# Kernel tuning notes

Hardware: AMD Instinct MI355X
Metric: run time of the kernel (lower is better)

Reference implementation:

```python
import jax, jax.numpy as jnp
import numpy as np

IN_FEATURES = 4096
OUT_FEATURES = 4096
N_TOKENS = 4096  # batch*seq rows fed through the linear layer


def setup_inputs() -> dict:
    key = jax.random.key(0)
    kx, kw, kb = jax.random.split(key, 3)
    x = jax.random.normal(kx, (N_TOKENS, IN_FEATURES), dtype=jnp.float32)
    # kaiming_uniform-like init scale for weight, uniform bias as in reset_parameters
    bound_w = float(np.sqrt(6.0 / ((1.0 + 5.0) * IN_FEATURES)))  # kaiming_uniform a=sqrt(5)
    weight = jax.random.uniform(kw, (OUT_FEATURES, IN_FEATURES), dtype=jnp.float32,
                                minval=-bound_w, maxval=bound_w)
    bound_b = float(1.0 / np.sqrt(IN_FEATURES))
    bias = jax.random.uniform(kb, (OUT_FEATURES,), dtype=jnp.float32,
                              minval=-bound_b, maxval=bound_b)
    return {"x": x, "weight": weight, "bias": bias}


def reference(x, weight, bias):
    # quantize_weights(bits=8): scale = 127 / max|W|; W_int8 = int8-cast(W*scale)
    # (numpy int8 cast truncates toward zero). The cutlass int8 GEMM computes
    # x_int8 @ W_int8^T, dequantized by 1/scale, plus bias. Math equivalent:
    # y = x @ (trunc(W*scale)/scale)^T + bias
    scale = 127.0 / jnp.max(jnp.abs(weight))
    w_q = jnp.clip(jnp.trunc(weight * scale), -127.0, 127.0)  # emulated int8 weight
    w_deq = w_q / scale                                       # [out, in]
    return jnp.einsum('ti,oi->to', x, w_deq) + bias           # [tokens, out]
```

## Files before the change

### kernel.cpp

```cpp
#include <hip/hip_runtime.h>
#include <stdint.h>

#define M_DIM 4096
#define N_DIM 4096
#define K_DIM 4096

typedef int i32x4 __attribute__((ext_vector_type(4)));

__global__ void prep1_kernel(const float* __restrict__ w,
                             const float* __restrict__ x,
                             float* __restrict__ wpmax,
                             char* __restrict__ xq,
                             float* __restrict__ xsinv) {
    __shared__ float sred[4];
    const int t = threadIdx.x;
    if (blockIdx.x < 2048) {
        int tid = blockIdx.x * 256 + t;
        const int stride = 2048 * 256;
        const int n4 = (N_DIM * K_DIM) / 4;
        const float4* w4 = (const float4*)w;
        float m = 0.f;
        for (int i = tid; i < n4; i += stride) {
            float4 a = w4[i];
            m = fmaxf(m, fmaxf(fmaxf(fabsf(a.x), fabsf(a.y)), fmaxf(fabsf(a.z), fabsf(a.w))));
        }
        for (int off = 32; off > 0; off >>= 1) m = fmaxf(m, __shfl_xor(m, off));
        if ((t & 63) == 0) sred[t >> 6] = m;
        __syncthreads();
        if (t == 0)
            wpmax[blockIdx.x] = fmaxf(fmaxf(sred[0], sred[1]), fmaxf(sred[2], sred[3]));
    } else {
        const int rbase = (blockIdx.x - 2048) * 2;
        #pragma unroll
        for (int r = 0; r < 2; ++r) {
            const int row = rbase + r;
            const float4* xr = (const float4*)(x + (size_t)row * K_DIM);
            float4 v[4];
            float m = 0.f;
            #pragma unroll
            for (int i = 0; i < 4; ++i) {
                v[i] = xr[t * 4 + i];
                m = fmaxf(m, fmaxf(fmaxf(fabsf(v[i].x), fabsf(v[i].y)),
                                   fmaxf(fabsf(v[i].z), fabsf(v[i].w))));
            }
            for (int off = 32; off > 0; off >>= 1) m = fmaxf(m, __shfl_xor(m, off));
            if ((t & 63) == 0) sred[t >> 6] = m;
            __syncthreads();
            m = fmaxf(fmaxf(fmaxf(sred[0], sred[1]), fmaxf(sred[2], sred[3])), 1e-30f);
            if (t == 0) xsinv[row] = m * (1.0f / 127.0f);
            const float scale = 127.0f / m;
            int4 o;
            int* op = (int*)&o;
            #pragma unroll
            for (int i = 0; i < 4; ++i) {
                int a = (int)rintf(v[i].x * scale);
                int b = (int)rintf(v[i].y * scale);
                int c = (int)rintf(v[i].z * scale);
                int d = (int)rintf(v[i].w * scale);
                op[i] = (a & 0xff) | ((b & 0xff) << 8) | ((c & 0xff) << 16) | (d << 24);
            }
            *(int4*)(xq + (size_t)row * K_DIM + t * 16) = o;
            __syncthreads();
        }
    }
}

__global__ void prep2_kernel(const float* __restrict__ w,
                             const float* __restrict__ wpmax,
                             int* __restrict__ wq4,
                             float* __restrict__ wdq_out) {
    __shared__ float sred[4];
    const int t = threadIdx.x;
    float m = 0.f;
    #pragma unroll
    for (int i = 0; i < 8; ++i) m = fmaxf(m, wpmax[t * 8 + i]);
    for (int off = 32; off > 0; off >>= 1) m = fmaxf(m, __shfl_xor(m, off));
    if ((t & 63) == 0) sred[t >> 6] = m;
    __syncthreads();
    const float maxv = fmaxf(fmaxf(sred[0], sred[1]), fmaxf(sred[2], sred[3]));
    const float wscale = 127.0f / maxv;
    if (blockIdx.x == 0 && t == 0) *wdq_out = maxv * (1.0f / 127.0f);

    int tid = blockIdx.x * 256 + t;
    const int stride = 2048 * 256;
    const int n4 = (N_DIM * K_DIM) / 4;
    const float4* w4 = (const float4*)w;
    for (int i = tid; i < n4; i += stride) {
        float4 a = w4[i];
        int w0 = (int)fminf(fmaxf(truncf(a.x * wscale), -127.f), 127.f);
        int w1 = (int)fminf(fmaxf(truncf(a.y * wscale), -127.f), 127.f);
        int w2 = (int)fminf(fmaxf(truncf(a.z * wscale), -127.f), 127.f);
        int w3 = (int)fminf(fmaxf(truncf(a.w * wscale), -127.f), 127.f);
        wq4[i] = (w0 & 0xff) | ((w1 & 0xff) << 8) | ((w2 & 0xff) << 16) | (w3 << 24);
    }
}

#define BAR()   __builtin_amdgcn_s_barrier()
#define FENCE() __builtin_amdgcn_sched_barrier(0)

#define MFMA_I8(ACC, AF, BF) \
    asm("v_mfma_i32_16x16x64_i8 %0, %1, %2, %0" : "+v"(ACC) : "v"(AF), "v"(BF))

__global__ __launch_bounds__(512, 2) void gemm_i8(
    const char* __restrict__ A,
    const char* __restrict__ B,
    const float* __restrict__ wdqp,
    const float* __restrict__ xsinv,
    const float* __restrict__ bias,
    float* __restrict__ C)
{
    __shared__ __align__(16) char sM[131072];

    int bid = (blockIdx.x & 7) * 32 + (blockIdx.x >> 3);
    const int bm = bid >> 4;
    const int bn = bid & 15;

    const int t    = threadIdx.x;
    const int wave = t >> 6;
    const int lane = t & 63;
    const int wm   = wave >> 2;
    const int wn   = wave & 3;

    i32x4 acc[2][2][4][2] = {};

    const int chunk = (((lane >> 4) << 4) ^ ((lane & 7) << 4));
    const int lbA0 = ((lane & 15) << 7) + chunk + wm * 8192;
    const int lbA1 = lbA0 ^ 64;
    const int lbB0 = ((lane & 15) << 7) + chunk + wn * 4096 + 65536;
    const int lbB1 = lbB0 ^ 64;

    const int srow = t >> 3;
    const int cch  = (t & 7) ^ (srow & 7);
    const char* Abase = A + (size_t)(bm * 256 + srow) * K_DIM + cch * 16;
    const char* Bbase = B + (size_t)(bn * 256 + srow) * K_DIM + cch * 16;
    const int wave_lds = wave * 1024;

#define STAGE(SRC, REG, H, KT, BUF) do {                                                \
        const char* _s = SRC + (H) * (128 * K_DIM) + ((KT) << 7);                       \
        char* _d = sM + (REG) + (BUF) * 32768 + (H) * 16384 + wave_lds;                 \
        __builtin_amdgcn_global_load_lds(                                               \
            (const __attribute__((address_space(1))) void*)_s,                          \
            (__attribute__((address_space(3))) void*)_d, 16, 0, 0);                     \
        __builtin_amdgcn_global_load_lds(                                               \
            (const __attribute__((address_space(1))) void*)(_s + (size_t)64 * K_DIM),   \
            (__attribute__((address_space(3))) void*)(_d + 8192), 16, 0, 0);            \
    } while(0)

#define LDA(H, BUF, AF) do {                                                            \
        _Pragma("unroll") for (int mi = 0; mi < 4; ++mi) {                              \
            AF[mi][0] = *(const i32x4*)(sM + (BUF)*32768 + (H)*16384 + mi*2048 + lbA0); \
            AF[mi][1] = *(const i32x4*)(sM + (BUF)*32768 + (H)*16384 + mi*2048 + lbA1); \
        }                                                                               \
    } while(0)

#define LDB(G, BUF, BF) do {                                                            \
        _Pragma("unroll") for (int ni = 0; ni < 2; ++ni) {                              \
            BF[ni][0] = *(const i32x4*)(sM + (BUF)*32768 + (G)*16384 + ni*2048 + lbB0); \
            BF[ni][1] = *(const i32x4*)(sM + (BUF)*32768 + (G)*16384 + ni*2048 + lbB1); \
        }                                                                               \
    } while(0)

#define MMAQ(H, G, AF, BF)                                                              \
        _Pragma("unroll") for (int kk = 0; kk < 2; ++kk)                                \
        _Pragma("unroll") for (int mi = 0; mi < 4; ++mi)                                \
        _Pragma("unroll") for (int ni = 0; ni < 2; ++ni)                                \
            MFMA_I8(acc[H][G][mi][ni], AF[mi][kk], BF[ni][kk]);

#define TILE(BUF, OBUF, KN) do {                                                        \
        LDA(0, BUF, af0); LDB(0, BUF, bf0);                    \
        FENCE();                                                                        \
        LDB(1, BUF, bf1);                                                  \
        STAGE(Abase, 0,     0, KN, OBUF);                                               \
        STAGE(Bbase, 65536, 0, KN, OBUF);                                               \
        STAGE(Abase, 0,     1, KN, OBUF);                                               \
        STAGE(Bbase, 65536, 1, KN, OBUF);                                               \
        LDA(1, BUF, af1);                                                  \
        FENCE();                                                                        \
        __builtin_amdgcn_s_setprio(1);                                                  \
        MMAQ(0, 0, af0, bf0);                                                           \
        MMAQ(0, 1, af0, bf1);                                                           \
        MMAQ(1, 1, af1, bf1);                                                           \
        MMAQ(1, 0, af1, bf0);                                                           \
        __builtin_amdgcn_s_setprio(0);                                                  \
        asm volatile("s_waitcnt vmcnt(0)");              \
        BAR();                                                                          \
        FENCE();                                                                        \
    } while(0)

    STAGE(Abase, 0,     0, 0, 0);
    STAGE(Bbase, 65536, 0, 0, 0);
    STAGE(Abase, 0,     1, 0, 0);
    STAGE(Bbase, 65536, 1, 0, 0);
    asm volatile("s_waitcnt vmcnt(0)");
    BAR();
    FENCE();

    i32x4 af0[4][2], af1[4][2], bf0[2][2], bf1[2][2];

    for (int it = 0; it < 16; ++it) {
        TILE(0, 1, (2 * it + 1) & 31);
        TILE(1, 0, (2 * it + 2) & 31);
    }

    const float wdq = *wdqp;

    #pragma unroll
    for (int h = 0; h < 2; ++h)
    #pragma unroll
    for (int mi = 0; mi < 4; ++mi) {
        const int grow0 = bm * 256 + h * 128 + wm * 64 + mi * 16 + (lane >> 4) * 4;
        float rs[4];
        #pragma unroll
        for (int rg = 0; rg < 4; ++rg) rs[rg] = xsinv[grow0 + rg] * wdq;
        #pragma unroll
        for (int g = 0; g < 2; ++g)
        #pragma unroll
        for (int ni = 0; ni < 2; ++ni) {
            const int gcol = bn * 256 + g * 128 + wn * 32 + ni * 16 + (lane & 15);
            const float bv = bias[gcol];
            #pragma unroll
            for (int rg = 0; rg < 4; ++rg)
                C[(size_t)(grow0 + rg) * N_DIM + gcol] =
                    (float)acc[h][g][mi][ni][rg] * rs[rg] + bv;
        }
    }

#undef STAGE
#undef LDA
#undef LDB
#undef MMAQ
#undef TILE
}

extern "C" void kernel_launch(void* const* d_in, const int* in_sizes, int n_in,
                              void* d_out, int out_size, void* d_ws, size_t ws_size,
                              hipStream_t stream) {
    const float* x    = (const float*)d_in[0];
    const float* w    = (const float*)d_in[1];
    const float* bias = (const float*)d_in[2];
    float* out = (float*)d_out;

    float* wpmax = (float*)d_ws;
    float* wdqp  = (float*)((char*)d_ws + 8192);
    float* xsinv = (float*)((char*)d_ws + 8448);
    char*  xq    = (char*)d_ws + 32768;
    char*  wq    = (char*)d_ws + 32768 + (size_t)M_DIM * K_DIM;

    prep1_kernel<<<4096, 256, 0, stream>>>(w, x, wpmax, xq, xsinv);
    prep2_kernel<<<2048, 256, 0, stream>>>(w, wpmax, (int*)wq, wdqp);

    const int grid = (M_DIM / 256) * (N_DIM / 256);
    gemm_i8<<<grid, 512, 0, stream>>>(xq, wq, wdqp, xsinv, bias, out);
}
```

Baseline: 101.1 us.

## Shrink GEMM tile to 128x256x64 with smaller LDS buffers for higher occupancy

Reworks the int8 GEMM tile from 256x256 with K-step 128 to 128x256 with K-step 64. LDS drops from 128KB to 48KB and launch bounds rise to 4 blocks per CU, so more blocks can be resident and latency is hidden better, and the grid doubles to 512 blocks. The LDS swizzle, staging and fragment-load patterns are rewritten for 64-byte rows. In exchange, each block reuses its data less, global traffic per FLOP goes up, and the K loop runs twice as many barrier-separated steps.

```diff
diff --git a/kernel.cpp b/kernel.cpp
--- a/kernel.cpp
+++ b/kernel.cpp
@@ -101,7 +101,9 @@
 #define MFMA_I8(ACC, AF, BF) \
     asm("v_mfma_i32_16x16x64_i8 %0, %1, %2, %0" : "+v"(ACC) : "v"(AF), "v"(BF))
 
-__global__ __launch_bounds__(512, 2) void gemm_i8(
+#define BUFSZ 24576
+
+__global__ __launch_bounds__(512, 4) void gemm_i8(
     const char* __restrict__ A,
     const char* __restrict__ B,
     const float* __restrict__ wdqp,
@@ -109,9 +111,9 @@
     const float* __restrict__ bias,
     float* __restrict__ C)
 {
-    __shared__ __align__(16) char sM[131072];
-
-    int bid = (blockIdx.x & 7) * 32 + (blockIdx.x >> 3);
+    __shared__ __align__(16) char sM[2 * BUFSZ];
+
+    int bid = (blockIdx.x & 7) * 64 + (blockIdx.x >> 3);
     const int bm = bid >> 4;
     const int bn = bid & 15;
 
@@ -121,114 +123,87 @@
     const int wm   = wave >> 2;
     const int wn   = wave & 3;
 
-    i32x4 acc[2][2][4][2] = {};
-
-    const int chunk = (((lane >> 4) << 4) ^ ((lane & 7) << 4));
-    const int lbA0 = ((lane & 15) << 7) + chunk + wm * 8192;
-    const int lbA1 = lbA0 ^ 64;
-    const int lbB0 = ((lane & 15) << 7) + chunk + wn * 4096 + 65536;
-    const int lbB1 = lbB0 ^ 64;
-
-    const int srow = t >> 3;
-    const int cch  = (t & 7) ^ (srow & 7);
-    const char* Abase = A + (size_t)(bm * 256 + srow) * K_DIM + cch * 16;
+    i32x4 acc[4][4] = {};
+
+    const int chunk = (((lane >> 4) ^ ((lane >> 1) & 3)) << 4);
+    const int lbA = ((lane & 15) << 6) + chunk + wm * 4096;
+    const int lbB = ((lane & 15) << 6) + chunk + wn * 4096 + 8192;
+
+    const int srow = t >> 2;
+    const int cch  = (t & 3) ^ ((t >> 3) & 3);
+    const char* Abase = A + (size_t)(bm * 128 + srow) * K_DIM + cch * 16;
     const char* Bbase = B + (size_t)(bn * 256 + srow) * K_DIM + cch * 16;
     const int wave_lds = wave * 1024;
 
-#define STAGE(SRC, REG, H, KT, BUF) do {                                                \
-        const char* _s = SRC + (H) * (128 * K_DIM) + ((KT) << 7);                       \
-        char* _d = sM + (REG) + (BUF) * 32768 + (H) * 16384 + wave_lds;                 \
+#define STAGE(KT, BUF) do {                                                             \
+        const char* _sa = Abase + ((KT) << 6);                                          \
+        char* _da = sM + (BUF) * BUFSZ + wave_lds;                                      \
         __builtin_amdgcn_global_load_lds(                                               \
-            (const __attribute__((address_space(1))) void*)_s,                          \
-            (__attribute__((address_space(3))) void*)_d, 16, 0, 0);                     \
+            (const __attribute__((address_space(1))) void*)_sa,                         \
+            (__attribute__((address_space(3))) void*)_da, 16, 0, 0);                    \
+        const char* _sb = Bbase + ((KT) << 6);                                          \
+        char* _db = sM + (BUF) * BUFSZ + 8192 + wave_lds;                               \
         __builtin_amdgcn_global_load_lds(                                               \
-            (const __attribute__((address_space(1))) void*)(_s + (size_t)64 * K_DIM),   \
-            (__attribute__((address_space(3))) void*)(_d + 8192), 16, 0, 0);            \
+            (const __attribute__((address_space(1))) void*)_sb,                         \
+            (__attribute__((address_space(3))) void*)_db, 16, 0, 0);                    \
+        __builtin_amdgcn_global_load_lds(                                               \
+            (const __attribute__((address_space(1))) void*)(_sb + (size_t)128 * K_DIM), \
+            (__attribute__((address_space(3))) void*)(_db + 8192), 16, 0, 0);           \
     } while(0)
 
-#define LDA(H, BUF, AF) do {                                                            \
-        _Pragma("unroll") for (int mi = 0; mi < 4; ++mi) {                              \
-            AF[mi][0] = *(const i32x4*)(sM + (BUF)*32768 + (H)*16384 + mi*2048 + lbA0); \
-            AF[mi][1] = *(const i32x4*)(sM + (BUF)*32768 + (H)*16384 + mi*2048 + lbA1); \
-        }                                                                               \
+#define LDAB(BUF) do {                                                                  \
+        _Pragma("unroll") for (int mi = 0; mi < 4; ++mi)                                \
+            af[mi] = *(const i32x4*)(sM + (BUF)*BUFSZ + mi*1024 + lbA);                 \
+        _Pragma("unroll") for (int ni = 0; ni < 4; ++ni)                                \
+            bf[ni] = *(const i32x4*)(sM + (BUF)*BUFSZ + ni*1024 + lbB);                 \
     } while(0)
 
-#define LDB(G, BUF, BF) do {                                                            \
-        _Pragma("unroll") for (int ni = 0; ni < 2; ++ni) {                              \
-            BF[ni][0] = *(const i32x4*)(sM + (BUF)*32768 + (G)*16384 + ni*2048 + lbB0); \
-            BF[ni][1] = *(const i32x4*)(sM + (BUF)*32768 + (G)*16384 + ni*2048 + lbB1); \
-        }                                                                               \
-    } while(0)
-
-#define MMAQ(H, G, AF, BF)                                                              \
-        _Pragma("unroll") for (int kk = 0; kk < 2; ++kk)                                \
-        _Pragma("unroll") for (int mi = 0; mi < 4; ++mi)                                \
-        _Pragma("unroll") for (int ni = 0; ni < 2; ++ni)                                \
-            MFMA_I8(acc[H][G][mi][ni], AF[mi][kk], BF[ni][kk]);
-
 #define TILE(BUF, OBUF, KN) do {                                                        \
-        LDA(0, BUF, af0); LDB(0, BUF, bf0);                    \
-        FENCE();                                                                        \
-        LDB(1, BUF, bf1);                                                  \
-        STAGE(Abase, 0,     0, KN, OBUF);                                               \
-        STAGE(Bbase, 65536, 0, KN, OBUF);                                               \
-        STAGE(Abase, 0,     1, KN, OBUF);                                               \
-        STAGE(Bbase, 65536, 1, KN, OBUF);                                               \
-        LDA(1, BUF, af1);                                                  \
+        STAGE(KN, OBUF);                                                                \
+        LDAB(BUF);                                                                      \
         FENCE();                                                                        \
         __builtin_amdgcn_s_setprio(1);                                                  \
-        MMAQ(0, 0, af0, bf0);                                                           \
-        MMAQ(0, 1, af0, bf1);                                                           \
-        MMAQ(1, 1, af1, bf1);                                                           \
-        MMAQ(1, 0, af1, bf0);                                                           \
+        _Pragma("unroll") for (int mi = 0; mi < 4; ++mi)                                \
+        _Pragma("unroll") for (int ni = 0; ni < 4; ++ni)                                \
+            MFMA_I8(acc[mi][ni], af[mi], bf[ni]);                                       \
         __builtin_amdgcn_s_setprio(0);                                                  \
-        asm volatile("s_waitcnt vmcnt(0)");              \
+        asm volatile("s_waitcnt vmcnt(0)");                                             \
         BAR();                                                                          \
         FENCE();                                                                        \
     } while(0)
 
-    STAGE(Abase, 0,     0, 0, 0);
-    STAGE(Bbase, 65536, 0, 0, 0);
-    STAGE(Abase, 0,     1, 0, 0);
-    STAGE(Bbase, 65536, 1, 0, 0);
+    STAGE(0, 0);
     asm volatile("s_waitcnt vmcnt(0)");
     BAR();
     FENCE();
 
-    i32x4 af0[4][2], af1[4][2], bf0[2][2], bf1[2][2];
-
-    for (int it = 0; it < 16; ++it) {
-        TILE(0, 1, (2 * it + 1) & 31);
-        TILE(1, 0, (2 * it + 2) & 31);
+    i32x4 af[4], bf[4];
+
+    for (int it = 0; it < 32; ++it) {
+        TILE(0, 1, (2 * it + 1) & 63);
+        TILE(1, 0, (2 * it + 2) & 63);
     }
 
     const float wdq = *wdqp;
 
-    #pragma unroll
-    for (int h = 0; h < 2; ++h)
     #pragma unroll
     for (int mi = 0; mi < 4; ++mi) {
-        const int grow0 = bm * 256 + h * 128 + wm * 64 + mi * 16 + (lane >> 4) * 4;
+        const int grow0 = bm * 128 + wm * 64 + mi * 16 + (lane >> 4) * 4;
         float rs[4];
         #pragma unroll
         for (int rg = 0; rg < 4; ++rg) rs[rg] = xsinv[grow0 + rg] * wdq;
         #pragma unroll
-        for (int g = 0; g < 2; ++g)
-        #pragma unroll
-        for (int ni = 0; ni < 2; ++ni) {
-            const int gcol = bn * 256 + g * 128 + wn * 32 + ni * 16 + (lane & 15);
+        for (int ni = 0; ni < 4; ++ni) {
+            const int gcol = bn * 256 + wn * 64 + ni * 16 + (lane & 15);
             const float bv = bias[gcol];
             #pragma unroll
             for (int rg = 0; rg < 4; ++rg)
-                C[(size_t)(grow0 + rg) * N_DIM + gcol] =
-                    (float)acc[h][g][mi][ni][rg] * rs[rg] + bv;
+                C[(size_t)(grow0 + rg) * N_DIM + gcol] = (float)acc[mi][ni][rg] * rs[rg] + bv;
         }
     }
 
 #undef STAGE
-#undef LDA
-#undef LDB
-#undef MMAQ
+#undef LDAB
 #undef TILE
 }
 
@@ -249,6 +224,6 @@
     prep1_kernel<<<4096, 256, 0, stream>>>(w, x, wpmax, xq, xsinv);
     prep2_kernel<<<2048, 256, 0, stream>>>(w, wpmax, (int*)wq, wdqp);
 
-    const int grid = (M_DIM / 256) * (N_DIM / 256);
+    const int grid = (M_DIM / 128) * (N_DIM / 256);
     gemm_i8<<<grid, 512, 0, stream>>>(xq, wq, wdqp, xsinv, bias, out);
 }
```

Result: slower. 113.3 us, median of 2 (+12.0%).

## Switch int8 GEMM inner product to 32x32x32 MFMA tiles

Applied to the files above, without the earlier changes.

Replaces the 16x16x64 int8 MFMA with the 32x32x32 variant. The LDS fragment addressing and swizzle, the accumulator layout and the epilogue row mapping change to match the new output layout. The larger MFMA tile halves the number of MFMA issues and fragment loads per wave for the same work, which should improve operand reuse. The risk is bank conflicts under the new swizzle, a different MFMA throughput and latency profile, and a less coalesced epilogue store pattern.

```diff
diff --git a/kernel.cpp b/kernel.cpp
--- a/kernel.cpp
+++ b/kernel.cpp
@@ -5,7 +5,8 @@
 #define N_DIM 4096
 #define K_DIM 4096
 
-typedef int i32x4 __attribute__((ext_vector_type(4)));
+typedef int i32x4  __attribute__((ext_vector_type(4)));
+typedef int i32x16 __attribute__((ext_vector_type(16)));
 
 __global__ void prep1_kernel(const float* __restrict__ w,
                              const float* __restrict__ x,
@@ -98,8 +99,8 @@
 #define BAR()   __builtin_amdgcn_s_barrier()
 #define FENCE() __builtin_amdgcn_sched_barrier(0)
 
-#define MFMA_I8(ACC, AF, BF) \
-    asm("v_mfma_i32_16x16x64_i8 %0, %1, %2, %0" : "+v"(ACC) : "v"(AF), "v"(BF))
+#define MFMA32_I8(ACC, AF, BF) \
+    asm("v_mfma_i32_32x32x32_i8 %0, %1, %2, %0" : "+v"(ACC) : "v"(AF), "v"(BF))
 
 __global__ __launch_bounds__(512, 2) void gemm_i8(
     const char* __restrict__ A,
@@ -121,13 +122,11 @@
     const int wm   = wave >> 2;
     const int wn   = wave & 3;
 
-    i32x4 acc[2][2][4][2] = {};
-
-    const int chunk = (((lane >> 4) << 4) ^ ((lane & 7) << 4));
-    const int lbA0 = ((lane & 15) << 7) + chunk + wm * 8192;
-    const int lbA1 = lbA0 ^ 64;
-    const int lbB0 = ((lane & 15) << 7) + chunk + wn * 4096 + 65536;
-    const int lbB1 = lbB0 ^ 64;
+    i32x16 acc[2][2][2] = {};
+
+    const int chunk32 = (((lane >> 5) ^ (lane & 7)) << 4);
+    const int lbA = ((lane & 31) << 7) + chunk32 + wm * 8192;
+    const int lbB = ((lane & 31) << 7) + chunk32 + wn * 4096 + 65536;
 
     const int srow = t >> 3;
     const int cch  = (t & 7) ^ (srow & 7);
@@ -147,24 +146,21 @@
     } while(0)
 
 #define LDA(H, BUF, AF) do {                                                            \
-        _Pragma("unroll") for (int mi = 0; mi < 4; ++mi) {                              \
-            AF[mi][0] = *(const i32x4*)(sM + (BUF)*32768 + (H)*16384 + mi*2048 + lbA0); \
-            AF[mi][1] = *(const i32x4*)(sM + (BUF)*32768 + (H)*16384 + mi*2048 + lbA1); \
-        }                                                                               \
+        _Pragma("unroll") for (int mt = 0; mt < 2; ++mt)                                \
+        _Pragma("unroll") for (int kk = 0; kk < 4; ++kk)                                \
+            AF[mt][kk] = *(const i32x4*)(sM + (BUF)*32768 + (H)*16384 + mt*4096         \
+                                            + (lbA ^ (kk << 5)));                      \
     } while(0)
 
 #define LDB(G, BUF, BF) do {                                                            \
-        _Pragma("unroll") for (int ni = 0; ni < 2; ++ni) {                              \
-            BF[ni][0] = *(const i32x4*)(sM + (BUF)*32768 + (G)*16384 + ni*2048 + lbB0); \
-            BF[ni][1] = *(const i32x4*)(sM + (BUF)*32768 + (G)*16384 + ni*2048 + lbB1); \
-        }                                                                               \
+        _Pragma("unroll") for (int kk = 0; kk < 4; ++kk)                                \
+            BF[kk] = *(const i32x4*)(sM + (BUF)*32768 + (G)*16384 + (lbB ^ (kk << 5))); \
     } while(0)
 
 #define MMAQ(H, G, AF, BF)                                                              \
-        _Pragma("unroll") for (int kk = 0; kk < 2; ++kk)                                \
-        _Pragma("unroll") for (int mi = 0; mi < 4; ++mi)                                \
-        _Pragma("unroll") for (int ni = 0; ni < 2; ++ni)                                \
-            MFMA_I8(acc[H][G][mi][ni], AF[mi][kk], BF[ni][kk]);
+        _Pragma("unroll") for (int kk = 0; kk < 4; ++kk)                                \
+        _Pragma("unroll") for (int mt = 0; mt < 2; ++mt)                                \
+            MFMA32_I8(acc[H][G][mt], AF[mt][kk], BF[kk]);
 
 #define TILE(BUF, OBUF, KN) do {                                                        \
         LDA(0, BUF, af0); LDB(0, BUF, bf0);                    \
@@ -195,7 +191,7 @@
     BAR();
     FENCE();
 
-    i32x4 af0[4][2], af1[4][2], bf0[2][2], bf1[2][2];
+    i32x4 af0[2][4], af1[2][4], bf0[4], bf1[4];
 
     for (int it = 0; it < 16; ++it) {
         TILE(0, 1, (2 * it + 1) & 31);
@@ -207,21 +203,21 @@
     #pragma unroll
     for (int h = 0; h < 2; ++h)
     #pragma unroll
-    for (int mi = 0; mi < 4; ++mi) {
-        const int grow0 = bm * 256 + h * 128 + wm * 64 + mi * 16 + (lane >> 4) * 4;
-        float rs[4];
+    for (int mt = 0; mt < 2; ++mt) {
+        const int grow0 = bm * 256 + h * 128 + wm * 64 + mt * 32 + 4 * (lane >> 5);
+        float rs[16];
         #pragma unroll
-        for (int rg = 0; rg < 4; ++rg) rs[rg] = xsinv[grow0 + rg] * wdq;
+        for (int rg = 0; rg < 16; ++rg)
+            rs[rg] = xsinv[grow0 + (rg & 3) + 8 * (rg >> 2)] * wdq;
         #pragma unroll
-        for (int g = 0; g < 2; ++g)
-        #pragma unroll
-        for (int ni = 0; ni < 2; ++ni) {
-            const int gcol = bn * 256 + g * 128 + wn * 32 + ni * 16 + (lane & 15);
+        for (int g = 0; g < 2; ++g) {
+            const int gcol = bn * 256 + g * 128 + wn * 32 + (lane & 31);
             const float bv = bias[gcol];
             #pragma unroll
-            for (int rg = 0; rg < 4; ++rg)
-                C[(size_t)(grow0 + rg) * N_DIM + gcol] =
-                    (float)acc[h][g][mi][ni][rg] * rs[rg] + bv;
+            for (int rg = 0; rg < 16; ++rg) {
+                const int grow = grow0 + (rg & 3) + 8 * (rg >> 2);
+                C[(size_t)grow * N_DIM + gcol] = (float)acc[h][g][mt][rg] * rs[rg] + bv;
+            }
         }
     }
 
```

Measured after the change: 112.9 us (median of 3 runs). 1.12x slower.

## Software-pipeline LDS fragment loads one tile ahead and keep accumulators in AGPRs

Applied to the files above, without the earlier changes.

The main loop now double-buffers the register fragments: each tile loads all A/B fragments for the current LDS buffer while the MFMAs run on fragments loaded in the previous iteration, with a prologue and an epilogue MMASET. The MFMA accumulator constraint moves from VGPRs to AGPRs to free VGPRs for the doubled fragment set. The aim is to hide LDS read latency behind matrix math. The cost is more register pressure at 2 blocks/CU, and possible copies between AGPRs and VGPRs in the epilogue.

```diff
diff --git a/kernel.cpp b/kernel.cpp
--- a/kernel.cpp
+++ b/kernel.cpp
@@ -99,7 +99,7 @@
 #define FENCE() __builtin_amdgcn_sched_barrier(0)
 
 #define MFMA_I8(ACC, AF, BF) \
-    asm("v_mfma_i32_16x16x64_i8 %0, %1, %2, %0" : "+v"(ACC) : "v"(AF), "v"(BF))
+    asm("v_mfma_i32_16x16x64_i8 %0, %1, %2, %0" : "+a"(ACC) : "v"(AF), "v"(BF))
 
 __global__ __launch_bounds__(512, 2) void gemm_i8(
     const char* __restrict__ A,
@@ -146,46 +146,52 @@
             (__attribute__((address_space(3))) void*)(_d + 8192), 16, 0, 0);            \
     } while(0)
 
-#define LDA(H, BUF, AF) do {                                                            \
+#define LDALL(BUF, AF0, AF1, BF0, BF1) do {                                             \
         _Pragma("unroll") for (int mi = 0; mi < 4; ++mi) {                              \
-            AF[mi][0] = *(const i32x4*)(sM + (BUF)*32768 + (H)*16384 + mi*2048 + lbA0); \
-            AF[mi][1] = *(const i32x4*)(sM + (BUF)*32768 + (H)*16384 + mi*2048 + lbA1); \
+            AF0[mi][0] = *(const i32x4*)(sM + (BUF)*32768 + mi*2048 + lbA0);            \
+            AF0[mi][1] = *(const i32x4*)(sM + (BUF)*32768 + mi*2048 + lbA1);            \
+            AF1[mi][0] = *(const i32x4*)(sM + (BUF)*32768 + 16384 + mi*2048 + lbA0);    \
+            AF1[mi][1] = *(const i32x4*)(sM + (BUF)*32768 + 16384 + mi*2048 + lbA1);    \
         }                                                                               \
-    } while(0)
-
-#define LDB(G, BUF, BF) do {                                                            \
         _Pragma("unroll") for (int ni = 0; ni < 2; ++ni) {                              \
-            BF[ni][0] = *(const i32x4*)(sM + (BUF)*32768 + (G)*16384 + ni*2048 + lbB0); \
-            BF[ni][1] = *(const i32x4*)(sM + (BUF)*32768 + (G)*16384 + ni*2048 + lbB1); \
+            BF0[ni][0] = *(const i32x4*)(sM + (BUF)*32768 + ni*2048 + lbB0);            \
+            BF0[ni][1] = *(const i32x4*)(sM + (BUF)*32768 + ni*2048 + lbB1);            \
+            BF1[ni][0] = *(const i32x4*)(sM + (BUF)*32768 + 16384 + ni*2048 + lbB0);    \
+            BF1[ni][1] = *(const i32x4*)(sM + (BUF)*32768 + 16384 + ni*2048 + lbB1);    \
         }                                                                               \
     } while(0)
 
-#define MMAQ(H, G, AF, BF)                                                              \
+#define MMASET(AF0, AF1, BF0, BF1) do {                                                 \
+        __builtin_amdgcn_s_setprio(1);                                                  \
         _Pragma("unroll") for (int kk = 0; kk < 2; ++kk)                                \
         _Pragma("unroll") for (int mi = 0; mi < 4; ++mi)                                \
-        _Pragma("unroll") for (int ni = 0; ni < 2; ++ni)                                \
-            MFMA_I8(acc[H][G][mi][ni], AF[mi][kk], BF[ni][kk]);
-
-#define TILE(BUF, OBUF, KN) do {                                                        \
-        LDA(0, BUF, af0); LDB(0, BUF, bf0);                    \
-        FENCE();                                                                        \
-        LDB(1, BUF, bf1);                                                  \
+        _Pragma("unroll") for (int ni = 0; ni < 2; ++ni) {                              \
+            MFMA_I8(acc[0][0][mi][ni], AF0[mi][kk], BF0[ni][kk]);                       \
+            MFMA_I8(acc[0][1][mi][ni], AF0[mi][kk], BF1[ni][kk]);                       \
+            MFMA_I8(acc[1][1][mi][ni], AF1[mi][kk], BF1[ni][kk]);                       \
+            MFMA_I8(acc[1][0][mi][ni], AF1[mi][kk], BF0[ni][kk]);                       \
+        }                                                                               \
+        __builtin_amdgcn_s_setprio(0);                                                  \
+    } while(0)
+
+#define TBODY(BUF, OBUF, KN, CA0, CA1, CB0, CB1, PA0, PA1, PB0, PB1) do {               \
+        LDALL(BUF, CA0, CA1, CB0, CB1);                \
+        FENCE();                                                                        \
         STAGE(Abase, 0,     0, KN, OBUF);                                               \
         STAGE(Bbase, 65536, 0, KN, OBUF);                                               \
         STAGE(Abase, 0,     1, KN, OBUF);                                               \
-        STAGE(Bbase, 65536, 1, KN, OBUF);                                               \
-        LDA(1, BUF, af1);                                                  \
-        FENCE();                                                                        \
-        __builtin_amdgcn_s_setprio(1);                                                  \
-        MMAQ(0, 0, af0, bf0);                                                           \
-        MMAQ(0, 1, af0, bf1);                                                           \
-        MMAQ(1, 1, af1, bf1);                                                           \
-        MMAQ(1, 0, af1, bf0);                                                           \
-        __builtin_amdgcn_s_setprio(0);                                                  \
-        asm volatile("s_waitcnt vmcnt(0)");              \
+        STAGE(Bbase, 65536, 1, KN, OBUF);                              \
+        FENCE();                                                                        \
+        MMASET(PA0, PA1, PB0, PB1);              \
+        FENCE();                                                                        \
+        asm volatile("s_waitcnt lgkmcnt(0)");    \
+        asm volatile("s_waitcnt vmcnt(0)");                     \
         BAR();                                                                          \
         FENCE();                                                                        \
     } while(0)
+
+    i32x4 pa0[4][2], pa1[4][2], pb0[2][2], pb1[2][2];
+    i32x4 qa0[4][2], qa1[4][2], qb0[2][2], qb1[2][2];
 
     STAGE(Abase, 0,     0, 0, 0);
     STAGE(Bbase, 65536, 0, 0, 0);
@@ -194,13 +200,23 @@
     asm volatile("s_waitcnt vmcnt(0)");
     BAR();
     FENCE();
-
-    i32x4 af0[4][2], af1[4][2], bf0[2][2], bf1[2][2];
-
-    for (int it = 0; it < 16; ++it) {
-        TILE(0, 1, (2 * it + 1) & 31);
-        TILE(1, 0, (2 * it + 2) & 31);
-    }
+    LDALL(0, pa0, pa1, pb0, pb1);
+    FENCE();
+    STAGE(Abase, 0,     0, 1, 1);
+    STAGE(Bbase, 65536, 0, 1, 1);
+    STAGE(Abase, 0,     1, 1, 1);
+    STAGE(Bbase, 65536, 1, 1, 1);
+    asm volatile("s_waitcnt lgkmcnt(0)");
+    asm volatile("s_waitcnt vmcnt(0)");
+    BAR();
+    FENCE();
+
+    TBODY(1, 0, 2, qa0, qa1, qb0, qb1, pa0, pa1, pb0, pb1);
+    for (int it = 1; it < 16; ++it) {
+        TBODY(0, 1, (2 * it + 1) & 31, pa0, pa1, pb0, pb1, qa0, qa1, qb0, qb1);
+        TBODY(1, 0, (2 * it + 2) & 31, qa0, qa1, qb0, qb1, pa0, pa1, pb0, pb1);
+    }
+    MMASET(qa0, qa1, qb0, qb1);
 
     const float wdq = *wdqp;
 
@@ -226,10 +242,9 @@
     }
 
 #undef STAGE
-#undef LDA
-#undef LDB
-#undef MMAQ
-#undef TILE
+#undef LDALL
+#undef MMASET
+#undef TBODY
 }
 
 extern "C" void kernel_launch(void* const* d_in, const int* in_sizes, int n_in,
```

Result: slower. 322.4 us (+218.9%).
